# Performance work log

Measured on AMD Instinct MI355X. Metric: run time of the kernel, lower is better.

The kernel has to match this reference:

```python
import jax, jax.numpy as jnp
import numpy as np

N, E, F_IN, H, H2, G, C = 30000, 480000, 1280, 512, 256, 64, 10


def _linear_init(key, fan_in, fan_out):
    k1, k2 = jax.random.split(key)
    s = 1.0 / np.sqrt(fan_in)
    W = jax.random.uniform(k1, (fan_in, fan_out), jnp.float32, -s, s)
    b = jax.random.uniform(k2, (fan_out,), jnp.float32, -s, s)
    return W, b


def setup_inputs() -> dict:
    key = jax.random.key(0)
    ks = jax.random.split(key, 6)
    x = jax.random.normal(ks[0], (N, F_IN), jnp.float32)
    edge_index = jax.random.randint(ks[1], (2, E), 0, N, dtype=jnp.int32).astype(jnp.int64)
    batch = jnp.sort(jax.random.randint(ks[2], (N,), 0, G, dtype=jnp.int32)).astype(jnp.int64)
    W1, b1 = _linear_init(ks[3], F_IN, H)
    beta2 = jnp.ones((), jnp.float32)  # AGNNConv beta init = 1.0 (trainable in prop2)
    W2, b2 = _linear_init(ks[4], H, H2)
    W3, b3 = _linear_init(ks[5], 2 * H2, C)
    return {"x": x, "edge_index": edge_index, "batch": batch,
            "W1": W1, "b1": b1, "beta2": beta2,
            "W2": W2, "b2": b2, "W3": W3, "b3": b3}


def _agnn(x, src, dst, beta, n):
    # L2 normalize (PyG F.normalize: clamp norm at 1e-12)
    norm = jnp.maximum(jnp.linalg.norm(x, axis=-1, keepdims=True), 1e-12)
    xn = x / norm
    # per-edge cosine similarity attention logits
    alpha = beta * jnp.sum(xn[src] * xn[dst], axis=-1)  # [E']
    # softmax over incoming edges of each destination node
    amax = jax.ops.segment_max(alpha, dst, num_segments=n)
    ex = jnp.exp(alpha - amax[dst])
    denom = jax.ops.segment_sum(ex, dst, num_segments=n)
    w = ex / denom[dst]
    # weighted scatter-add of raw source features
    return jax.ops.segment_sum(w[:, None] * x[src], dst, num_segments=n)


def reference(x, edge_index, batch, W1, b1, beta2, W2, b2, W3, b3):
    n = x.shape[0]
    h = jax.nn.relu(x @ W1 + b1)  # [N, 512]
    # AGNNConv adds self-loops by default
    loops = jnp.arange(n, dtype=edge_index.dtype)
    src = jnp.concatenate([edge_index[0], loops])
    dst = jnp.concatenate([edge_index[1], loops])
    h = _agnn(h, src, dst, jnp.float32(1.0), n)  # prop1: fixed beta=1
    h = _agnn(h, src, dst, beta2, n)             # prop2: learned beta
    h = jax.nn.relu(h @ W2 + b2)  # [N, 256]
    # global max / mean pool per graph
    gmx = jax.ops.segment_max(h, batch, num_segments=G)
    cnt = jnp.maximum(jax.ops.segment_sum(jnp.ones((n,), h.dtype), batch, num_segments=G), 1.0)
    gav = jax.ops.segment_sum(h, batch, num_segments=G) / cnt[:, None]
    return jnp.concatenate([gmx, gav], axis=1) @ W3 + b3  # [G, C]
```

## Files before the change

kernel.cpp:

```cpp
#include <hip/hip_runtime.h>
#include <hip/hip_bf16.h>
#include <cstdint>


typedef __attribute__((ext_vector_type(8))) short bf16x8;
typedef __attribute__((ext_vector_type(4))) float f32x4;
typedef __attribute__((ext_vector_type(8))) unsigned short ushort8;
typedef __attribute__((ext_vector_type(4))) unsigned short ushort4v;
typedef __attribute__((ext_vector_type(4))) unsigned int uint4v;

#define WAITV(n) asm volatile("s_waitcnt vmcnt(" #n ")" ::: "memory")
#define WAITLGKM asm volatile("s_waitcnt lgkmcnt(0)" ::: "memory")

__device__ inline unsigned short f2bf(float f) {
    unsigned int u = __float_as_uint(f);
    u += 0x7FFFu + ((u >> 16) & 1u);
    return (unsigned short)(u >> 16);
}

__device__ __forceinline__ float bf2f(unsigned short u) {
    return __uint_as_float(((unsigned int)u) << 16);
}

__device__ __forceinline__ unsigned int cvtpk(float lo, float hi) {
    unsigned int r;
    asm("v_cvt_pk_bf16_f32 %0, %1, %2" : "=v"(r) : "v"(lo), "v"(hi));
    return r;
}

__device__ __forceinline__ void gload_lds16(const void* g, void* l) {
    __builtin_amdgcn_global_load_lds(
        (const __attribute__((address_space(1))) void*)g,
        (__attribute__((address_space(3))) void*)l, 16, 0, 0);
}

__device__ __forceinline__ float wave_sum_dpp(float p) {
    int t;
    t = __builtin_amdgcn_update_dpp(0, __float_as_int(p), 0xB1, 0xf, 0xf, true);
    p += __int_as_float(t);
    t = __builtin_amdgcn_update_dpp(0, __float_as_int(p), 0x4E, 0xf, 0xf, true);
    p += __int_as_float(t);
    t = __builtin_amdgcn_update_dpp(0, __float_as_int(p), 0x141, 0xf, 0xf, true);
    p += __int_as_float(t);
    t = __builtin_amdgcn_update_dpp(0, __float_as_int(p), 0x140, 0xf, 0xf, true);
    p += __int_as_float(t);
    t = __builtin_amdgcn_update_dpp(0, __float_as_int(p), 0x142, 0xf, 0xf, true);
    p += __int_as_float(t);
    t = __builtin_amdgcn_update_dpp(0, __float_as_int(p), 0x143, 0xf, 0xf, true);
    p += __int_as_float(t);
    return __int_as_float(__builtin_amdgcn_readlane(__float_as_int(p), 63));
}

__global__ __launch_bounds__(256) void k_transpose_bf16(
    const float* __restrict__ W, unsigned short* __restrict__ Wt, int K, int N) {
    __shared__ unsigned short t[32][33];
    int k0 = blockIdx.x * 32, n0 = blockIdx.y * 32;
    int tr = threadIdx.x >> 3;
    int tc = (threadIdx.x & 7) * 4;
    float4 v = *(const float4*)(W + (long)(k0 + tr) * N + n0 + tc);
    t[tr][tc + 0] = f2bf(v.x); t[tr][tc + 1] = f2bf(v.y);
    t[tr][tc + 2] = f2bf(v.z); t[tr][tc + 3] = f2bf(v.w);
    __syncthreads();
    ushort4v o = { t[tc + 0][tr], t[tc + 1][tr], t[tc + 2][tr], t[tc + 3][tr] };
    *(ushort4v*)(Wt + (long)(n0 + tr) * K + k0 + tc) = o;
}

template <int K, int BN, int NOUT, bool AF32, bool OUTBF16>
__global__ __launch_bounds__(512, 4) void k_gemm_bias_relu(
    const void* __restrict__ Av, const unsigned short* __restrict__ Bt,
    const float* __restrict__ bias, void* __restrict__ Cv, int M) {
    constexpr int NS = K / 32;
    __shared__ unsigned short As[3][128 * 32];
    __shared__ unsigned short Bs[3][BN * 32];
    int tid = threadIdx.x;
    int w = tid >> 6, l = tid & 63;
    int wm = w >> 2, wn = w & 3;
    int mBase = blockIdx.x * 128;
    int nBase = blockIdx.y * BN;

    const float* Af = (const float*)Av;
    const unsigned short* Ab = (const unsigned short*)Av;

    int arow = tid >> 2;
    int aslot = (tid & 3) ^ ((arow >> 1) & 3);
    long aRowG = mBase + arow; if (aRowG >= M) aRowG = M - 1;
    const float* aptr = AF32 ? (Af + aRowG * K + (tid & 3) * 8) : nullptr;

    auto stageB = [&](int b, int k0) {
#pragma unroll
        for (int o = 0; o < BN / 128; ++o) {
            int rbase = (w * (BN / 128) + o) * 16;
            int row = rbase + (l >> 2);
            int gsrc = (l & 3) ^ ((row >> 1) & 3);
            gload_lds16(Bt + (long)(nBase + row) * K + k0 + gsrc * 8,
                        &Bs[b][rbase * 32]);
        }
    };
    auto stageAbf = [&](int b, int k0) {
        int rbase = w * 16;
        int row = rbase + (l >> 2);
        int gsrc = (l & 3) ^ ((row >> 1) & 3);
        long gr = mBase + row; if (gr >= M) gr = M - 1;
        gload_lds16(Ab + gr * K + k0 + gsrc * 8, &As[b][rbase * 32]);
    };
    auto loadA = [&](int k0, float4& u0, float4& u1) {
        u0 = *(const float4*)(aptr + k0);
        u1 = *(const float4*)(aptr + k0 + 4);
    };
    auto writeA = [&](int b, float4 u0, float4 u1) {
        uint4v p = { cvtpk(u0.x, u0.y), cvtpk(u0.z, u0.w),
                     cvtpk(u1.x, u1.y), cvtpk(u1.z, u1.w) };
        *(uint4v*)(&As[b][arow * 32 + aslot * 8]) = p;
    };

    f32x4 acc[4][4] = {};
    float4 curA0 = {}, curA1 = {}, nxtA0 = {}, nxtA1 = {};

    if constexpr (AF32) {
        float4 z0, z1;
        loadA(0, z0, z1);
        stageB(0, 0);
        loadA(32, curA0, curA1);
        stageB(1, 32);
        writeA(0, z0, z1);
    } else {
        stageAbf(0, 0); stageB(0, 0);
        stageAbf(1, 32); stageB(1, 32);
    }
    WAITLGKM;

#pragma unroll
    for (int t = 0; t < NS; ++t) {
        const int cb = t % 3, nb = (t + 1) % 3, fb = (t + 2) % 3;
        __builtin_amdgcn_s_barrier();
        __builtin_amdgcn_sched_barrier(0);
        if constexpr (AF32) {
            if (t + 2 < NS) {
                loadA((t + 2) * 32, nxtA0, nxtA1);
                stageB(fb, (t + 2) * 32);
            }
            if (t + 1 < NS) {
                writeA(nb, curA0, curA1);
                curA0 = nxtA0; curA1 = nxtA1;
            }
            if (t < NS - 2) { WAITV(6); }
            else if (t == NS - 2) { WAITV(2); }
            else { WAITV(0); }
        } else {
            if (t + 2 < NS) {
                stageAbf(fb, (t + 2) * 32);
                stageB(fb, (t + 2) * 32);
            }
            if (t < NS - 2) { WAITV(6); }
            else if (t == NS - 2) { WAITV(3); }
            else { WAITV(0); }
        }
        __builtin_amdgcn_sched_barrier(0);
        bf16x8 af[4];
#pragma unroll
        for (int m = 0; m < 4; ++m) {
            int ra = wm * 64 + m * 16 + (l & 15);
            int g = (l >> 4) ^ ((ra >> 1) & 3);
            af[m] = *(const bf16x8*)(&As[cb][ra * 32 + g * 8]);
        }
#pragma unroll
        for (int n = 0; n < 4; ++n) {
            int rb = wn * 64 + n * 16 + (l & 15);
            int g = (l >> 4) ^ ((rb >> 1) & 3);
            bf16x8 bfr = *(const bf16x8*)(&Bs[cb][rb * 32 + g * 8]);
#pragma unroll
            for (int m = 0; m < 4; ++m)
                acc[m][n] = __builtin_amdgcn_mfma_f32_16x16x32_bf16(
                    af[m], bfr, acc[m][n], 0, 0, 0);
        }
    }

#pragma unroll
    for (int m = 0; m < 4; ++m) {
        int row = mBase + wm * 64 + m * 16 + (l >> 4) * 4;
#pragma unroll
        for (int n = 0; n < 4; ++n) {
            int colg = nBase + wn * 64 + n * 16 + (l & 15);
            float bv = bias[colg];
#pragma unroll
            for (int r = 0; r < 4; ++r) {
                if (row + r < M) {
                    float v = fmaxf(acc[m][n][r] + bv, 0.f);
                    if constexpr (OUTBF16)
                        ((unsigned short*)Cv)[(long)(row + r) * NOUT + colg] = f2bf(v);
                    else
                        ((float*)Cv)[(long)(row + r) * NOUT + colg] = v;
                }
            }
        }
    }
}

__global__ void k_csr_init(int* __restrict__ cnt, int* __restrict__ fill, int n) {
    int i = blockIdx.x * blockDim.x + threadIdx.x;
    if (i < n) { cnt[i] = 1; fill[i] = 0; }
}

__global__ void k_csr_count(const int* __restrict__ ei, int* __restrict__ cnt, int E) {
    int e = blockIdx.x * blockDim.x + threadIdx.x;
    if (e < E) atomicAdd(&cnt[ei[E + e]], 1);
}

__global__ __launch_bounds__(1024) void k_scan1(const int* __restrict__ cnt,
                                                int* __restrict__ rowp,
                                                int* __restrict__ bsum, int n) {
    __shared__ int wsum[16];
    int b = blockIdx.x, t = threadIdx.x, lane = t & 63, w = t >> 6;
    int i = b * 1024 + t;
    int v = (i < n) ? cnt[i] : 0;
    int x = v;
#pragma unroll
    for (int off = 1; off < 64; off <<= 1) {
        int y = __shfl_up(x, off, 64);
        if (lane >= off) x += y;
    }
    if (lane == 63) wsum[w] = x;
    __syncthreads();
    if (t < 16) {
        int s = wsum[t];
#pragma unroll
        for (int off = 1; off < 16; off <<= 1) {
            int y = __shfl_up(s, off, 64);
            if (t >= off) s += y;
        }
        wsum[t] = s;
    }
    __syncthreads();
    int wo = w ? wsum[w - 1] : 0;
    if (i < n) rowp[i] = wo + x - v;
    if (t == 0) bsum[b] = wsum[15];
}

__global__ __launch_bounds__(64) void k_scan2(int* __restrict__ bsum, int nb) {
    int lane = threadIdx.x;
    int v = (lane < nb) ? bsum[lane] : 0;
    int x = v;
#pragma unroll
    for (int off = 1; off < 64; off <<= 1) {
        int y = __shfl_up(x, off, 64);
        if (lane >= off) x += y;
    }
    int total = __shfl(x, nb - 1, 64);
    if (lane < nb) bsum[lane] = x - v;
    if (lane == 0) bsum[nb] = total;
}

__global__ __launch_bounds__(1024) void k_scan3(const int* __restrict__ bsum,
                                                int* __restrict__ rowp, int n, int nb) {
    int i = blockIdx.x * 1024 + threadIdx.x;
    if (i < n) rowp[i] += bsum[i >> 10];
    else if (i == n) rowp[n] = bsum[nb];
}

__global__ void k_csr_fill(const int* __restrict__ ei, const int* __restrict__ rowp,
                           int* __restrict__ fill, int* __restrict__ col, int E, int n) {
    int idx = blockIdx.x * blockDim.x + threadIdx.x;
    if (idx < E) {
        int d = ei[E + idx];
        int s = ei[idx];
        int pos = atomicAdd(&fill[d], 1);
        col[rowp[d] + pos] = s;
    } else if (idx < E + n) {
        int nd = idx - E;
        int pos = atomicAdd(&fill[nd], 1);
        col[rowp[nd] + pos] = nd;
    }
}

__global__ __launch_bounds__(256) void k_norm_bf16(const unsigned short* __restrict__ h,
                                                   float* __restrict__ invn, int n) {
    int row = blockIdx.x * 4 + (threadIdx.x >> 6);
    int lane = threadIdx.x & 63;
    if (row >= n) return;
    ushort8 v = *(const ushort8*)(h + (long)row * 512 + lane * 8);
    float s = 0.f;
#pragma unroll
    for (int e = 0; e < 8; ++e) { float f = bf2f(v[e]); s += f * f; }
    s = wave_sum_dpp(s);
    if (lane == 0) invn[row] = 1.f / fmaxf(sqrtf(s), 1e-12f);
}

__global__ __launch_bounds__(256) void k_agnn(
    const unsigned short* __restrict__ h, const float* __restrict__ invn,
    const int* __restrict__ rowp, const int* __restrict__ col,
    const float* __restrict__ beta_ptr, unsigned short* __restrict__ out,
    float* __restrict__ invn_out, int nNodes) {
    int dst = blockIdx.x * 4 + (threadIdx.x >> 6);
    int lane = threadIdx.x & 63;
    if (dst >= nNodes) return;
    float beta = beta_ptr ? beta_ptr[0] : 1.0f;
    ushort8 hdv = *(const ushort8*)(h + (long)dst * 512 + lane * 8);
    float hd[8];
#pragma unroll
    for (int e = 0; e < 8; ++e) hd[e] = bf2f(hdv[e]);
    float coef = beta * invn[dst];
    int s0 = rowp[dst], s1 = rowp[dst + 1];

    float m = -1e30f, ssum = 0.f;
    float acc[8] = {0.f, 0.f, 0.f, 0.f, 0.f, 0.f, 0.f, 0.f};

    for (int base = s0; base < s1; base += 64) {
        int cnt = min(s1 - base, 64);
        int gi = base + lane; if (gi >= s1) gi = s1 - 1;
        int idxl = col[gi];
        float vinl = invn[idxl];
        int src0 = __builtin_amdgcn_readlane(idxl, 0);
        ushort8 nxt = *(const ushort8*)(h + (long)src0 * 512 + lane * 8);
        for (int j = 0; j < cnt; ++j) {
            ushort8 cur = nxt;
            if (j + 1 < cnt) {
                int sn = __builtin_amdgcn_readlane(idxl, j + 1);
                nxt = *(const ushort8*)(h + (long)sn * 512 + lane * 8);
            }
            float a[8];
#pragma unroll
            for (int e = 0; e < 8; ++e) a[e] = bf2f(cur[e]);
            float p = a[0] * hd[0] + a[1] * hd[1] + a[2] * hd[2] + a[3] * hd[3] +
                      a[4] * hd[4] + a[5] * hd[5] + a[6] * hd[6] + a[7] * hd[7];
            p = wave_sum_dpp(p);
            float vin_j = __int_as_float(
                __builtin_amdgcn_readlane(__float_as_int(vinl), j));
            float alpha = coef * vin_j * p;
            if (alpha > m) {
                float sc = __expf(m - alpha);
                ssum *= sc;
#pragma unroll
                for (int e = 0; e < 8; ++e) acc[e] *= sc;
                m = alpha;
            }
            float wgt = __expf(alpha - m);
            ssum += wgt;
#pragma unroll
            for (int e = 0; e < 8; ++e) acc[e] += wgt * a[e];
        }
    }
    float inv_s = 1.f / ssum;
#pragma unroll
    for (int e = 0; e < 8; ++e) acc[e] *= inv_s;

    uint4v o = { cvtpk(acc[0], acc[1]), cvtpk(acc[2], acc[3]),
                 cvtpk(acc[4], acc[5]), cvtpk(acc[6], acc[7]) };
    *(uint4v*)(out + (long)dst * 512 + lane * 8) = o;

    if (invn_out) {
        float s = 0.f;
#pragma unroll
        for (int e = 0; e < 8; ++e) s += acc[e] * acc[e];
        s = wave_sum_dpp(s);
        if (lane == 0) invn_out[dst] = 1.f / fmaxf(sqrtf(s), 1e-12f);
    }
}

__global__ void k_bounds(const int* __restrict__ batch, int* __restrict__ starts,
                         int n, int G) {
    int g = blockIdx.x * blockDim.x + threadIdx.x;
    if (g > G) return;
    int lo = 0, hi = n;
    while (lo < hi) {
        int mid = (lo + hi) >> 1;
        if (batch[mid] < g) lo = mid + 1; else hi = mid;
    }
    starts[g] = lo;
}

__global__ __launch_bounds__(256) void k_pool(const float* __restrict__ h3,
                                              const int* __restrict__ starts,
                                              float* __restrict__ pooled) {
    int g = blockIdx.x;
    int t = threadIdx.x;
    int s = starts[g], e = starts[g + 1];
    float mx = -3.402823466e38f, sm = 0.f;
    int r = s;
    for (; r + 4 <= e; r += 4) {
        float v0 = h3[(long)(r + 0) * 256 + t];
        float v1 = h3[(long)(r + 1) * 256 + t];
        float v2 = h3[(long)(r + 2) * 256 + t];
        float v3 = h3[(long)(r + 3) * 256 + t];
        mx = fmaxf(mx, fmaxf(fmaxf(v0, v1), fmaxf(v2, v3)));
        sm += (v0 + v1) + (v2 + v3);
    }
    for (; r < e; ++r) {
        float v = h3[(long)r * 256 + t];
        mx = fmaxf(mx, v); sm += v;
    }
    float cnt = fmaxf((float)(e - s), 1.f);
    pooled[g * 512 + t] = mx;
    pooled[g * 512 + 256 + t] = sm / cnt;
}

__global__ __launch_bounds__(64) void k_final(const float* __restrict__ pooled,
                                              const float* __restrict__ W3,
                                              const float* __restrict__ b3,
                                              float* __restrict__ out, int C) {
    int g = blockIdx.x;
    int lane = threadIdx.x;
    for (int c = 0; c < C; c++) {
        float p = 0.f;
        for (int k = lane; k < 512; k += 64) p += pooled[g * 512 + k] * W3[k * C + c];
#pragma unroll
        for (int off = 32; off; off >>= 1) p += __shfl_xor(p, off, 64);
        if (lane == 0) out[g * C + c] = p + b3[c];
    }
}

extern "C" void kernel_launch(void* const* d_in, const int* in_sizes, int n_in,
                              void* d_out, int out_size, void* d_ws, size_t ws_size,
                              hipStream_t stream) {
    const float* x     = (const float*)d_in[0];
    const int*   ei    = (const int*)d_in[1];
    const int*   batch = (const int*)d_in[2];
    const float* W1    = (const float*)d_in[3];
    const float* b1    = (const float*)d_in[4];
    const float* beta2 = (const float*)d_in[5];
    const float* W2    = (const float*)d_in[6];
    const float* b2    = (const float*)d_in[7];
    const float* W3    = (const float*)d_in[8];
    const float* b3    = (const float*)d_in[9];
    float* out = (float*)d_out;

    const int N = in_sizes[2];
    const int E = in_sizes[1] / 2;
    const int F_IN = in_sizes[0] / N;
    const int H = in_sizes[4];
    const int H2 = in_sizes[7];
    const int C = in_sizes[9];
    const int G = out_size / C;

    char* ws = (char*)d_ws;
    unsigned short* H1B = (unsigned short*)(ws + 0);
    unsigned short* HPB = (unsigned short*)(ws + 31000000L);
    unsigned short* H2B = (unsigned short*)(ws + 62000000L);
    float*          H3  = (float*)(ws + 0);
    unsigned short* W1T = (unsigned short*)(ws + 93000000L);
    unsigned short* W2T = (unsigned short*)(ws + 94500000L);
    float* INVN_A = (float*)(ws + 95000000L);
    float* INVN_B = (float*)(ws + 95200000L);
    int*   CNT    = (int*)(ws + 95400000L);
    int*   FILL   = (int*)(ws + 95600000L);
    int*   ROWP   = (int*)(ws + 95800000L);
    int*   COL    = (int*)(ws + 96000000L);
    int*   BSUM   = (int*)(ws + 98100000L);
    int*   START  = (int*)(ws + 98110000L);
    float* POOLED = (float*)(ws + 98120000L);

    { dim3 g1(F_IN / 32, H / 32); k_transpose_bf16<<<g1, 256, 0, stream>>>(W1, W1T, F_IN, H); }
    { dim3 g2(H / 32, H2 / 32);   k_transpose_bf16<<<g2, 256, 0, stream>>>(W2, W2T, H, H2); }

    int nb = (N + 1023) / 1024;
    k_csr_init<<<(N + 255) / 256, 256, 0, stream>>>(CNT, FILL, N);
    k_csr_count<<<(E + 255) / 256, 256, 0, stream>>>(ei, CNT, E);
    k_scan1<<<nb, 1024, 0, stream>>>(CNT, ROWP, BSUM, N);
    k_scan2<<<1, 64, 0, stream>>>(BSUM, nb);
    k_scan3<<<(N + 1 + 1023) / 1024, 1024, 0, stream>>>(BSUM, ROWP, N, nb);
    k_csr_fill<<<(E + N + 255) / 256, 256, 0, stream>>>(ei, ROWP, FILL, COL, E, N);

    {
        dim3 grid((N + 127) / 128, H / 256);
        k_gemm_bias_relu<1280, 256, 512, true, true>
            <<<grid, 512, 0, stream>>>(x, W1T, b1, H1B, N);
    }

    k_norm_bf16<<<(N + 3) / 4, 256, 0, stream>>>(H1B, INVN_A, N);
    k_agnn<<<(N + 3) / 4, 256, 0, stream>>>(H1B, INVN_A, ROWP, COL, nullptr, HPB, INVN_B, N);

    k_agnn<<<(N + 3) / 4, 256, 0, stream>>>(HPB, INVN_B, ROWP, COL, beta2, H2B, nullptr, N);

    {
        dim3 grid((N + 127) / 128, 1);
        k_gemm_bias_relu<512, 256, 256, false, false>
            <<<grid, 512, 0, stream>>>(H2B, W2T, b2, H3, N);
    }

    k_bounds<<<1, 128, 0, stream>>>(batch, START, N, G);
    k_pool<<<G, 256, 0, stream>>>(H3, START, POOLED);
    k_final<<<G, 64, 0, stream>>>(POOLED, W3, b3, out, C);
}
```

Before: 375.3 us.

## Deepen GEMM software pipeline: prefetch A three stages ahead, move waits after compute

Restructures the GEMM main loop so the global loads of fp32 A are issued three k-steps ahead using two alternating register sets. Loads and B staging for future stages are issued before the MFMA compute of the current stage, and the vmcnt wait plus barrier move after the compute. This hides global load latency behind the matrix math and removes the barrier-then-wait stall at the top of each iteration. The cost is more live registers, which may lower occupancy, and a more fragile waitcnt accounting.

```diff
diff --git a/kernel.cpp b/kernel.cpp
--- a/kernel.cpp
+++ b/kernel.cpp
@@ -11,6 +11,7 @@
 
 #define WAITV(n) asm volatile("s_waitcnt vmcnt(" #n ")" ::: "memory")
 #define WAITLGKM asm volatile("s_waitcnt lgkmcnt(0)" ::: "memory")
+#define SCHEDB __builtin_amdgcn_sched_barrier(0)
 
 __device__ inline unsigned short f2bf(float f) {
     unsigned int u = __float_as_uint(f);
@@ -112,50 +113,7 @@
                      cvtpk(u1.x, u1.y), cvtpk(u1.z, u1.w) };
         *(uint4v*)(&As[b][arow * 32 + aslot * 8]) = p;
     };
-
-    f32x4 acc[4][4] = {};
-    float4 curA0 = {}, curA1 = {}, nxtA0 = {}, nxtA1 = {};
-
-    if constexpr (AF32) {
-        float4 z0, z1;
-        loadA(0, z0, z1);
-        stageB(0, 0);
-        loadA(32, curA0, curA1);
-        stageB(1, 32);
-        writeA(0, z0, z1);
-    } else {
-        stageAbf(0, 0); stageB(0, 0);
-        stageAbf(1, 32); stageB(1, 32);
-    }
-    WAITLGKM;
-
-#pragma unroll
-    for (int t = 0; t < NS; ++t) {
-        const int cb = t % 3, nb = (t + 1) % 3, fb = (t + 2) % 3;
-        __builtin_amdgcn_s_barrier();
-        __builtin_amdgcn_sched_barrier(0);
-        if constexpr (AF32) {
-            if (t + 2 < NS) {
-                loadA((t + 2) * 32, nxtA0, nxtA1);
-                stageB(fb, (t + 2) * 32);
-            }
-            if (t + 1 < NS) {
-                writeA(nb, curA0, curA1);
-                curA0 = nxtA0; curA1 = nxtA1;
-            }
-            if (t < NS - 2) { WAITV(6); }
-            else if (t == NS - 2) { WAITV(2); }
-            else { WAITV(0); }
-        } else {
-            if (t + 2 < NS) {
-                stageAbf(fb, (t + 2) * 32);
-                stageB(fb, (t + 2) * 32);
-            }
-            if (t < NS - 2) { WAITV(6); }
-            else if (t == NS - 2) { WAITV(3); }
-            else { WAITV(0); }
-        }
-        __builtin_amdgcn_sched_barrier(0);
+    auto compute = [&](int cb, f32x4 (&acc)[4][4]) {
         bf16x8 af[4];
 #pragma unroll
         for (int m = 0; m < 4; ++m) {
@@ -172,6 +130,60 @@
             for (int m = 0; m < 4; ++m)
                 acc[m][n] = __builtin_amdgcn_mfma_f32_16x16x32_bf16(
                     af[m], bfr, acc[m][n], 0, 0, 0);
+        }
+    };
+
+    f32x4 acc[4][4] = {};
+    float4 Ra0 = {}, Ra1 = {}, Rb0 = {}, Rb1 = {};
+
+    if constexpr (AF32) {
+        loadA(0, Ra0, Ra1);
+        stageB(0, 0);
+        loadA(32, Rb0, Rb1);
+        stageB(1, 32);
+        writeA(0, Ra0, Ra1);
+        if (NS > 2) loadA(64, Ra0, Ra1);
+        WAITV(6);
+    } else {
+        stageAbf(0, 0); stageB(0, 0);
+        stageAbf(1, 32); stageB(1, 32);
+        WAITV(3);
+    }
+    WAITLGKM;
+    SCHEDB;
+    __builtin_amdgcn_s_barrier();
+
+#pragma unroll
+    for (int t = 0; t < NS; ++t) {
+        const int cb = t % 3, nb = (t + 1) % 3, fb = (t + 2) % 3;
+        if constexpr (AF32) {
+            if (t + 2 < NS) stageB(fb, (t + 2) * 32);
+            if (t + 1 < NS) {
+                if ((t & 1) == 0) writeA(nb, Rb0, Rb1);
+                else              writeA(nb, Ra0, Ra1);
+            }
+            if (t + 3 < NS) {
+                if ((t & 1) == 0) loadA((t + 3) * 32, Rb0, Rb1);
+                else              loadA((t + 3) * 32, Ra0, Ra1);
+            }
+        } else {
+            if (t + 2 < NS) { stageAbf(fb, (t + 2) * 32); stageB(fb, (t + 2) * 32); }
+        }
+        SCHEDB;
+        compute(cb, acc);
+        if (t < NS - 1) {
+            if constexpr (AF32) {
+                if (t + 3 < NS)      { WAITV(4); }
+                else if (t + 2 < NS) { WAITV(2); }
+                else                 { WAITV(0); }
+            } else {
+                if (t + 2 < NS)      { WAITV(3); }
+                else                 { WAITV(0); }
+            }
+            WAITLGKM;
+            SCHEDB;
+            __builtin_amdgcn_s_barrier();
+            SCHEDB;
         }
     }
 
```

Result: slower. 383.6 us (+2.2%).
